# Optimization experiments

Measured on AMD Instinct MI355X. Metric: run time of the kernel, lower is better.

The kernel has to match this reference:

```python
import jax, jax.numpy as jnp
import numpy as np

B, C, N, D = 4, 128, 4096, 128  # batch, channels (=d_tran=out), points
BN_EPS = 1e-5


def setup_inputs() -> dict:
    key = jax.random.key(0)
    ks = jax.random.split(key, 10)
    s = 1.0 / np.sqrt(C)
    return {
        "x": jax.random.normal(ks[0], (B, C, N), dtype=jnp.float32),
        "Wqk": jax.random.uniform(ks[1], (D, C), minval=-s, maxval=s, dtype=jnp.float32),  # shared q/k weight
        "Wv": jax.random.uniform(ks[2], (D, C), minval=-s, maxval=s, dtype=jnp.float32),
        "bv": jax.random.uniform(ks[3], (D,), minval=-s, maxval=s, dtype=jnp.float32),
        "Wt": jax.random.uniform(ks[4], (C, D), minval=-s, maxval=s, dtype=jnp.float32),
        "bt": jax.random.uniform(ks[5], (C,), minval=-s, maxval=s, dtype=jnp.float32),
        "gamma": jnp.ones((C,), dtype=jnp.float32) + 0.1 * jax.random.normal(ks[6], (C,), dtype=jnp.float32),
        "beta": 0.1 * jax.random.normal(ks[7], (C,), dtype=jnp.float32),
        "rmean": 0.1 * jax.random.normal(ks[8], (C,), dtype=jnp.float32),
        "rvar": jax.random.uniform(ks[9], (C,), minval=0.5, maxval=1.5, dtype=jnp.float32),
    }


def reference(x, Wqk, Wv, bv, Wt, bt, gamma, beta, rmean, rvar):
    # x: [B, C, N]; 1x1 convs are per-point matmuls over the channel dim.
    x_q = jnp.einsum('dc,bcn->bnd', Wqk, x)                 # [B, N, D]
    x_k = jnp.einsum('dc,bcn->bdn', Wqk, x)                 # [B, D, N] (tied weight)
    x_v = jnp.einsum('dc,bcn->bdn', Wv, x) + bv[None, :, None]
    energy = jnp.einsum('bnd,bdm->bnm', x_q, x_k)           # [B, N, N]
    attention = jax.nn.softmax(energy, axis=-1)             # row softmax
    attention = attention / (1e-9 + attention.sum(axis=1, keepdims=True))  # L1 over columns
    x_r = jnp.einsum('bdn,bnm->bdm', x_v, attention)        # [B, D, N]
    y = jnp.einsum('od,bdn->bon', Wt, x - x_r) + bt[None, :, None]
    # BatchNorm1d, inference mode (running stats)
    y = gamma[None, :, None] * (y - rmean[None, :, None]) * jax.lax.rsqrt(rvar[None, :, None] + BN_EPS) + beta[None, :, None]
    return x + jax.nn.relu(y)
```

## Files before the change

kernel.cpp:

```cpp
#include <hip/hip_runtime.h>
#include <hip/hip_bf16.h>

typedef unsigned int u32;
typedef unsigned short u16;
using bf16x8 = __attribute__((ext_vector_type(8))) short;
using f32x4  = __attribute__((ext_vector_type(4))) float;
using f32x16 = __attribute__((ext_vector_type(16))) float;

#define B_ 4
#define C_ 128
#define N_ 4096
#define D_ 128
#define NS 8
#define NSEG (N_ / NS)

#define QS_STRIDE 136
#define VS_STRIDE 40

__device__ __forceinline__ u16 f2bf(float f) {
    u32 x = __builtin_bit_cast(u32, f);
    x = x + 0x7fffu + ((x >> 16) & 1u);
    return (u16)(x >> 16);
}
__device__ __forceinline__ float bf2f(u16 h) {
    return __builtin_bit_cast(float, (u32)h << 16);
}
__device__ __forceinline__ u32 cvtpk(float lo, float hi) {
    u32 d;
    asm("v_cvt_pk_bf16_f32 %0, %1, %2" : "=v"(d) : "v"(lo), "v"(hi));
    return d;
}
#define EXP2 __builtin_amdgcn_exp2f
__device__ __forceinline__ bf16x8 pack8(const float* v, float s) {
    bf16x8 r;
#pragma unroll
    for (int j = 0; j < 8; ++j) r[j] = (short)f2bf(v[j] * s);
    return r;
}

__global__ __launch_bounds__(256) void k_proj(
        const float* __restrict__ x, const float* __restrict__ Wqk,
        const float* __restrict__ Wv, const float* __restrict__ bv,
        u16* __restrict__ Qbf, u16* __restrict__ Vbf) {
    __shared__ float xs[C_ * 65];
    const int bid = blockIdx.x;
    const int b  = bid >> 6;
    const int n0 = (bid & 63) << 6;
    const int t  = threadIdx.x;
    const float* xb = x + (size_t)b * C_ * N_;
    for (int i = 0; i < 32; ++i) {
        int idx = i * 256 + t;
        int c = idx >> 6, n = idx & 63;
        xs[c * 65 + n] = xb[(size_t)c * N_ + n0 + n];
    }
    __syncthreads();
    const int lane = t & 63, w = t >> 6;
    const int l15 = lane & 15, g = lane >> 4;
    const float SC = 1.2011224087864498f;

    bf16x8 xf[4];
#pragma unroll
    for (int kk = 0; kk < 4; ++kk) {
        float tmp[8];
#pragma unroll
        for (int j = 0; j < 8; ++j) tmp[j] = xs[(kk * 32 + g * 8 + j) * 65 + (16 * w + l15)];
        xf[kk] = pack8(tmp, 1.0f);
    }
    for (int dt = 0; dt < 8; ++dt) {
        const int d = dt * 16 + l15;
        bf16x8 wq[4], wv[4];
#pragma unroll
        for (int kk = 0; kk < 4; ++kk) {
            const float* pq = Wqk + (size_t)d * C_ + kk * 32 + g * 8;
            const float* pv = Wv  + (size_t)d * C_ + kk * 32 + g * 8;
            float a[8], c8[8];
#pragma unroll
            for (int j = 0; j < 8; ++j) { a[j] = pq[j]; c8[j] = pv[j]; }
            wq[kk] = pack8(a, SC);
            wv[kk] = pack8(c8, 1.0f);
        }
        f32x4 aq = {0.f, 0.f, 0.f, 0.f}, av = {0.f, 0.f, 0.f, 0.f};
#pragma unroll
        for (int kk = 0; kk < 4; ++kk) {
            aq = __builtin_amdgcn_mfma_f32_16x16x32_bf16(xf[kk], wq[kk], aq, 0, 0, 0);
            av = __builtin_amdgcn_mfma_f32_16x16x32_bf16(wv[kk], xf[kk], av, 0, 0, 0);
        }
#pragma unroll
        for (int r = 0; r < 4; ++r) {
            int nn = n0 + 16 * w + g * 4 + r;
            Qbf[((size_t)b * N_ + nn) * D_ + dt * 16 + l15] = f2bf(aq[r]);
            int dd = dt * 16 + g * 4 + r;
            Vbf[((size_t)b * D_ + dd) * N_ + n0 + 16 * w + l15] = f2bf(av[r] + bv[dd]);
        }
    }
}

__global__ __launch_bounds__(256, 4) void k_pass1(const u16* __restrict__ Qbf,
                                                  float* __restrict__ rsp) {
    __shared__ __align__(16) u16 qs[32 * QS_STRIDE];
    int bid = blockIdx.x;
    const int s = bid & 7; bid >>= 3;
    const int ntile = bid & 31; const int b = bid >> 5;
    const int t = threadIdx.x, lane = t & 63, w = t >> 6;
    const int l31 = lane & 31, hi = lane >> 5;
    const int nb = ntile * 128 + w * 32;

    bf16x8 bqn[8];
    {
        const u16* qn = Qbf + ((size_t)b * N_ + nb + l31) * D_ + hi * 8;
#pragma unroll
        for (int dblk = 0; dblk < 8; ++dblk) bqn[dblk] = *(const bf16x8*)(qn + dblk * 16);
    }
    const int srow = t >> 4, sslot = t & 15;
    const u16* qsrc = Qbf + ((size_t)b * N_ + s * NSEG + srow) * D_ + sslot * 8;
    u16* qdst = qs + srow * QS_STRIDE + sslot * 8;
    uint4 qpre0 = *(const uint4*)qsrc;
    uint4 qpre1 = *(const uint4*)(qsrc + (size_t)16 * D_);

    float rs0 = 0.f, rs1 = 0.f;
    for (int mc = 0; mc < NSEG / 32; ++mc) {
        __syncthreads();
        *(uint4*)qdst = qpre0;
        *(uint4*)(qdst + 16 * QS_STRIDE) = qpre1;
        if (mc < NSEG / 32 - 1) {
            qpre0 = *(const uint4*)(qsrc + (size_t)(mc + 1) * 32 * D_);
            qpre1 = *(const uint4*)(qsrc + (size_t)((mc + 1) * 32 + 16) * D_);
        }
        __syncthreads();
        f32x16 e;
#pragma unroll
        for (int i = 0; i < 16; ++i) e[i] = 0.f;
#pragma unroll
        for (int dblk = 0; dblk < 8; ++dblk) {
            bf16x8 am = *(const bf16x8*)(qs + l31 * QS_STRIDE + (2 * dblk + hi) * 8);
            e = __builtin_amdgcn_mfma_f32_32x32x16_bf16(am, bqn[dblk], e, 0, 0, 0);
        }
#pragma unroll
        for (int r = 0; r < 16; r += 2) {
            rs0 += EXP2(e[r] - 64.0f);
            rs1 += EXP2(e[r + 1] - 64.0f);
        }
    }
    float rs = rs0 + rs1;
    rs += __shfl_xor(rs, 32);
    if (lane < 32) rsp[((size_t)s * B_ + b) * N_ + nb + l31] = rs;
}

__global__ void k_irs(const float* __restrict__ rsp, float* __restrict__ irs) {
    int i = blockIdx.x * 256 + threadIdx.x;
    if (i < B_ * N_) {
        float s = 0.f;
#pragma unroll
        for (int sp = 0; sp < NS; ++sp) s += rsp[(size_t)sp * B_ * N_ + i];
        irs[i] = 1.0f / s;
    }
}

__global__ __launch_bounds__(256, 3) void k_pass2(
        const u16* __restrict__ Qbf, const u16* __restrict__ Vbf,
        const float* __restrict__ irs, u32* __restrict__ Rp32,
        float* __restrict__ csp) {
    __shared__ __align__(16) u16 qs[32 * QS_STRIDE];
    __shared__ __align__(16) u16 vs[128 * VS_STRIDE];
    int bid = blockIdx.x;
    const int s = bid & 7; bid >>= 3;
    const int mtile = bid & 31; const int b = bid >> 5;
    const int t = threadIdx.x, lane = t & 63, w = t >> 6;
    const int l31 = lane & 31, hi = lane >> 5;
    const int m0 = mtile * 128 + w * 32;

    bf16x8 bq[8];
    {
        const u16* qm = Qbf + ((size_t)b * N_ + m0 + l31) * D_ + hi * 8;
#pragma unroll
        for (int dblk = 0; dblk < 8; ++dblk) bq[dblk] = *(const bf16x8*)(qm + dblk * 16);
    }
    f32x16 acc[4];
#pragma unroll
    for (int i = 0; i < 4; ++i)
#pragma unroll
        for (int r = 0; r < 16; ++r) acc[i][r] = 0.f;
    float cs = 0.f;
    const float* irsb = irs + (size_t)b * N_;

    const int qrow = t >> 4, qslot = t & 15;
    const u16* qsrc = Qbf + ((size_t)b * N_ + s * NSEG + qrow) * D_ + qslot * 8;
    u16* qdst = qs + qrow * QS_STRIDE + qslot * 8;
    const int vd = t >> 2, vslot = t & 3;
    const u16* vsrc = Vbf + ((size_t)b * D_ + vd) * N_ + s * NSEG + vslot * 8;
    u16* vdst = vs + vd * VS_STRIDE + vslot * 8;

    uint4 qpre0 = *(const uint4*)qsrc;
    uint4 qpre1 = *(const uint4*)(qsrc + (size_t)16 * D_);
    uint4 vpre0 = *(const uint4*)vsrc;
    uint4 vpre1 = *(const uint4*)(vsrc + (size_t)64 * N_);

    for (int nc = 0; nc < NSEG / 32; ++nc) {
        const int nb = s * NSEG + nc * 32;
        __syncthreads();
        *(uint4*)qdst = qpre0;
        *(uint4*)(qdst + 16 * QS_STRIDE) = qpre1;
        *(uint4*)vdst = vpre0;
        *(uint4*)(vdst + 64 * VS_STRIDE) = vpre1;
        if (nc < NSEG / 32 - 1) {
            qpre0 = *(const uint4*)(qsrc + (size_t)(nc + 1) * 32 * D_);
            qpre1 = *(const uint4*)(qsrc + (size_t)((nc + 1) * 32 + 16) * D_);
            vpre0 = *(const uint4*)(vsrc + (nc + 1) * 32);
            vpre1 = *(const uint4*)(vsrc + (size_t)64 * N_ + (nc + 1) * 32);
        }
        __syncthreads();

        const float* irp = irsb + nb;
        float si[32];
#pragma unroll
        for (int j = 0; j < 32; ++j) si[j] = irp[j];

        f32x16 e;
#pragma unroll
        for (int i = 0; i < 16; ++i) e[i] = 0.f;
#pragma unroll
        for (int dblk = 0; dblk < 8; ++dblk) {
            bf16x8 aq = *(const bf16x8*)(qs + l31 * QS_STRIDE + (2 * dblk + hi) * 8);
            e = __builtin_amdgcn_mfma_f32_32x32x16_bf16(aq, bq[dblk], e, 0, 0, 0);
        }
        uint4 bpA0, bpA1;
        {
            u32 A[8];
#pragma unroll
            for (int i = 0; i < 8; ++i) {
                const int c = 2 * (i & 1) + 8 * (i >> 1);
                float ir0 = hi ? si[c + 4] : si[c];
                float ir1 = hi ? si[c + 5] : si[c + 1];
                float p0 = EXP2(e[2 * i] - 64.0f) * ir0;
                float p1 = EXP2(e[2 * i + 1] - 64.0f) * ir1;
                cs += p0 + p1;
                A[i] = cvtpk(p0, p1);
            }
            u32 X0 = (u32)__shfl_xor((int)A[0], 32), X1 = (u32)__shfl_xor((int)A[1], 32);
            u32 X2 = (u32)__shfl_xor((int)A[2], 32), X3 = (u32)__shfl_xor((int)A[3], 32);
            u32 X4 = (u32)__shfl_xor((int)A[4], 32), X5 = (u32)__shfl_xor((int)A[5], 32);
            u32 X6 = (u32)__shfl_xor((int)A[6], 32), X7 = (u32)__shfl_xor((int)A[7], 32);
            bpA0 = (uint4){hi ? X2 : A[0], hi ? X3 : A[1], hi ? A[2] : X0, hi ? A[3] : X1};
            bpA1 = (uint4){hi ? X6 : A[4], hi ? X7 : A[5], hi ? A[6] : X4, hi ? A[7] : X5};
        }
#pragma unroll
        for (int nblk = 0; nblk < 2; ++nblk) {
            bf16x8 bp = __builtin_bit_cast(bf16x8, nblk ? bpA1 : bpA0);
#pragma unroll
            for (int dblk = 0; dblk < 4; ++dblk) {
                bf16x8 av = *(const bf16x8*)(vs + (dblk * 32 + l31) * VS_STRIDE +
                                             (nblk * 2 + hi) * 8);
                acc[dblk] = __builtin_amdgcn_mfma_f32_32x32x16_bf16(av, bp, acc[dblk], 0, 0, 0);
            }
        }
    }
    cs += __shfl_xor(cs, 32);
    if (lane < 32) csp[((size_t)s * B_ + b) * N_ + m0 + l31] = cs;
    u32* rpb = Rp32 + ((size_t)s * B_ + b) * (size_t)(D_ / 2) * N_;
#pragma unroll
    for (int dblk = 0; dblk < 4; ++dblk) {
#pragma unroll
        for (int j = 0; j < 8; ++j) {
            const int row = dblk * 16 + (j & 1) + 4 * (j >> 1) + 2 * hi;
            u32 pk = cvtpk(acc[dblk][2 * j], acc[dblk][2 * j + 1]);
            rpb[(size_t)row * N_ + m0 + l31] = pk;
        }
    }
}

__global__ __launch_bounds__(256) void k_final(
        const float* __restrict__ x, const float* __restrict__ Wt,
        const float* __restrict__ bt, const float* __restrict__ gamma,
        const float* __restrict__ beta, const float* __restrict__ rmean,
        const float* __restrict__ rvar, const u32* __restrict__ Rp32,
        const float* __restrict__ csp, float* __restrict__ out) {
    __shared__ float us[128 * 65];
    __shared__ float icss[64];
    const int bid = blockIdx.x;
    const int b = bid >> 6;
    const int n0 = (bid & 63) << 6;
    const int t = threadIdx.x, lane = t & 63, w = t >> 6;
    const int l15 = lane & 15, g = lane >> 4;
    if (t < 64) {
        float s = 0.f;
#pragma unroll
        for (int sp = 0; sp < NS; ++sp)
            s += csp[((size_t)sp * B_ + b) * N_ + n0 + t];
        icss[t] = 1.0f / (1e-9f + s);
    }
    __syncthreads();
    const float* xb = x + (size_t)b * C_ * N_;
    for (int i = 0; i < 16; ++i) {
        int idx = i * 256 + t;
        int dp = idx >> 6, n = idx & 63;
        float r0 = 0.f, r1 = 0.f;
#pragma unroll
        for (int sp = 0; sp < NS; ++sp) {
            u32 v = Rp32[(((size_t)(sp * B_ + b) * (D_ / 2)) + dp) * N_ + n0 + n];
            r0 += bf2f((u16)(v & 0xffffu));
            r1 += bf2f((u16)(v >> 16));
        }
        float ic = icss[n];
        us[(2 * dp) * 65 + n]     = xb[(size_t)(2 * dp) * N_ + n0 + n]     - r0 * ic;
        us[(2 * dp + 1) * 65 + n] = xb[(size_t)(2 * dp + 1) * N_ + n0 + n] - r1 * ic;
    }
    __syncthreads();
    bf16x8 uf[4];
#pragma unroll
    for (int kk = 0; kk < 4; ++kk) {
        float tmp[8];
#pragma unroll
        for (int j = 0; j < 8; ++j) tmp[j] = us[(kk * 32 + g * 8 + j) * 65 + (16 * w + l15)];
        uf[kk] = pack8(tmp, 1.0f);
    }
    for (int ct = 0; ct < 8; ++ct) {
        const int c = ct * 16 + l15;
        bf16x8 wf[4];
#pragma unroll
        for (int kk = 0; kk < 4; ++kk) {
            const float* p = Wt + (size_t)c * D_ + kk * 32 + g * 8;
            float a[8];
#pragma unroll
            for (int j = 0; j < 8; ++j) a[j] = p[j];
            wf[kk] = pack8(a, 1.0f);
        }
        f32x4 acc = {0.f, 0.f, 0.f, 0.f};
#pragma unroll
        for (int kk = 0; kk < 4; ++kk)
            acc = __builtin_amdgcn_mfma_f32_16x16x32_bf16(wf[kk], uf[kk], acc, 0, 0, 0);
#pragma unroll
        for (int r = 0; r < 4; ++r) {
            const int cc = ct * 16 + g * 4 + r;
            const int nn = n0 + 16 * w + l15;
            float y = acc[r] + bt[cc];
            float bn = gamma[cc] * (y - rmean[cc]) * rsqrtf(rvar[cc] + 1e-5f) + beta[cc];
            float rl = fmaxf(bn, 0.0f);
            out[((size_t)b * C_ + cc) * N_ + nn] = xb[(size_t)cc * N_ + nn] + rl;
        }
    }
}

extern "C" void kernel_launch(void* const* d_in, const int* in_sizes, int n_in,
                              void* d_out, int out_size, void* d_ws, size_t ws_size,
                              hipStream_t stream) {
    (void)in_sizes; (void)n_in; (void)out_size; (void)ws_size;
    const float* x     = (const float*)d_in[0];
    const float* Wqk   = (const float*)d_in[1];
    const float* Wv    = (const float*)d_in[2];
    const float* bv    = (const float*)d_in[3];
    const float* Wt    = (const float*)d_in[4];
    const float* bt    = (const float*)d_in[5];
    const float* gamma = (const float*)d_in[6];
    const float* beta  = (const float*)d_in[7];
    const float* rmean = (const float*)d_in[8];
    const float* rvar  = (const float*)d_in[9];
    float* out = (float*)d_out;

    char* ws = (char*)d_ws;
    u16*   Qbf = (u16*)(ws);
    u16*   Vbf = (u16*)(ws + 4194304);
    float* rsp = (float*)(ws + 8388608);
    float* irs = (float*)(ws + 8912896);
    float* csp = (float*)(ws + 8978432);
    u32*   Rp  = (u32*)(ws + 9502720);

    k_proj  <<<B_ * 64,      256, 0, stream>>>(x, Wqk, Wv, bv, Qbf, Vbf);
    k_pass1 <<<B_ * 32 * NS, 256, 0, stream>>>(Qbf, rsp);
    k_irs   <<<(B_ * N_ + 255) / 256, 256, 0, stream>>>(rsp, irs);
    k_pass2 <<<B_ * 32 * NS, 256, 0, stream>>>(Qbf, Vbf, irs, Rp, csp);
    k_final <<<B_ * 64,      256, 0, stream>>>(x, Wt, bt, gamma, beta, rmean, rvar, Rp, csp, out);
}
```

Measured before the change: 128.9 us.

## Double-buffer LDS tiles in attention passes, split MFMA chains, widen final kernel

```diff
diff --git a/kernel.cpp b/kernel.cpp
--- a/kernel.cpp
+++ b/kernel.cpp
@@ -97,7 +97,7 @@
 
 __global__ __launch_bounds__(256, 4) void k_pass1(const u16* __restrict__ Qbf,
                                                   float* __restrict__ rsp) {
-    __shared__ __align__(16) u16 qs[32 * QS_STRIDE];
+    __shared__ __align__(16) u16 qs[2][32 * QS_STRIDE];
     int bid = blockIdx.x;
     const int s = bid & 7; bid >>= 3;
     const int ntile = bid & 31; const int b = bid >> 5;
@@ -113,33 +113,44 @@
     }
     const int srow = t >> 4, sslot = t & 15;
     const u16* qsrc = Qbf + ((size_t)b * N_ + s * NSEG + srow) * D_ + sslot * 8;
-    u16* qdst = qs + srow * QS_STRIDE + sslot * 8;
-    uint4 qpre0 = *(const uint4*)qsrc;
-    uint4 qpre1 = *(const uint4*)(qsrc + (size_t)16 * D_);
+    const int qoff = srow * QS_STRIDE + sslot * 8;
+
+    {
+        uint4 a0 = *(const uint4*)qsrc;
+        uint4 a1 = *(const uint4*)(qsrc + (size_t)16 * D_);
+        *(uint4*)&qs[0][qoff] = a0;
+        *(uint4*)&qs[0][qoff + 16 * QS_STRIDE] = a1;
+    }
+    __syncthreads();
 
     float rs0 = 0.f, rs1 = 0.f;
     for (int mc = 0; mc < NSEG / 32; ++mc) {
-        __syncthreads();
-        *(uint4*)qdst = qpre0;
-        *(uint4*)(qdst + 16 * QS_STRIDE) = qpre1;
+        const int cur = mc & 1;
+        uint4 qpre0, qpre1;
         if (mc < NSEG / 32 - 1) {
             qpre0 = *(const uint4*)(qsrc + (size_t)(mc + 1) * 32 * D_);
             qpre1 = *(const uint4*)(qsrc + (size_t)((mc + 1) * 32 + 16) * D_);
         }
+        f32x16 ea, eb;
+#pragma unroll
+        for (int i = 0; i < 16; ++i) { ea[i] = 0.f; eb[i] = 0.f; }
+#pragma unroll
+        for (int dblk = 0; dblk < 4; ++dblk) {
+            bf16x8 am0 = *(const bf16x8*)(qs[cur] + l31 * QS_STRIDE + (2 * dblk + hi) * 8);
+            bf16x8 am1 = *(const bf16x8*)(qs[cur] + l31 * QS_STRIDE + (2 * (dblk + 4) + hi) * 8);
+            ea = __builtin_amdgcn_mfma_f32_32x32x16_bf16(am0, bqn[dblk], ea, 0, 0, 0);
+            eb = __builtin_amdgcn_mfma_f32_32x32x16_bf16(am1, bqn[dblk + 4], eb, 0, 0, 0);
+        }
+#pragma unroll
+        for (int r = 0; r < 16; r += 2) {
+            rs0 += EXP2(ea[r] + eb[r] - 64.0f);
+            rs1 += EXP2(ea[r + 1] + eb[r + 1] - 64.0f);
+        }
+        if (mc < NSEG / 32 - 1) {
+            *(uint4*)&qs[cur ^ 1][qoff] = qpre0;
+            *(uint4*)&qs[cur ^ 1][qoff + 16 * QS_STRIDE] = qpre1;
+        }
         __syncthreads();
-        f32x16 e;
-#pragma unroll
-        for (int i = 0; i < 16; ++i) e[i] = 0.f;
-#pragma unroll
-        for (int dblk = 0; dblk < 8; ++dblk) {
-            bf16x8 am = *(const bf16x8*)(qs + l31 * QS_STRIDE + (2 * dblk + hi) * 8);
-            e = __builtin_amdgcn_mfma_f32_32x32x16_bf16(am, bqn[dblk], e, 0, 0, 0);
-        }
-#pragma unroll
-        for (int r = 0; r < 16; r += 2) {
-            rs0 += EXP2(e[r] - 64.0f);
-            rs1 += EXP2(e[r + 1] - 64.0f);
-        }
     }
     float rs = rs0 + rs1;
     rs += __shfl_xor(rs, 32);
@@ -160,8 +171,8 @@
         const u16* __restrict__ Qbf, const u16* __restrict__ Vbf,
         const float* __restrict__ irs, u32* __restrict__ Rp32,
         float* __restrict__ csp) {
-    __shared__ __align__(16) u16 qs[32 * QS_STRIDE];
-    __shared__ __align__(16) u16 vs[128 * VS_STRIDE];
+    __shared__ __align__(16) u16 qs[2][32 * QS_STRIDE];
+    __shared__ __align__(16) u16 vs[2][128 * VS_STRIDE];
     int bid = blockIdx.x;
     const int s = bid & 7; bid >>= 3;
     const int mtile = bid & 31; const int b = bid >> 5;
@@ -185,43 +196,47 @@
 
     const int qrow = t >> 4, qslot = t & 15;
     const u16* qsrc = Qbf + ((size_t)b * N_ + s * NSEG + qrow) * D_ + qslot * 8;
-    u16* qdst = qs + qrow * QS_STRIDE + qslot * 8;
+    const int qoff = qrow * QS_STRIDE + qslot * 8;
     const int vd = t >> 2, vslot = t & 3;
     const u16* vsrc = Vbf + ((size_t)b * D_ + vd) * N_ + s * NSEG + vslot * 8;
-    u16* vdst = vs + vd * VS_STRIDE + vslot * 8;
-
-    uint4 qpre0 = *(const uint4*)qsrc;
-    uint4 qpre1 = *(const uint4*)(qsrc + (size_t)16 * D_);
-    uint4 vpre0 = *(const uint4*)vsrc;
-    uint4 vpre1 = *(const uint4*)(vsrc + (size_t)64 * N_);
+    const int voff = vd * VS_STRIDE + vslot * 8;
+
+    {
+        uint4 a0 = *(const uint4*)qsrc;
+        uint4 a1 = *(const uint4*)(qsrc + (size_t)16 * D_);
+        uint4 b0 = *(const uint4*)vsrc;
+        uint4 b1 = *(const uint4*)(vsrc + (size_t)64 * N_);
+        *(uint4*)&qs[0][qoff] = a0;
+        *(uint4*)&qs[0][qoff + 16 * QS_STRIDE] = a1;
+        *(uint4*)&vs[0][voff] = b0;
+        *(uint4*)&vs[0][voff + 64 * VS_STRIDE] = b1;
+    }
+    __syncthreads();
 
     for (int nc = 0; nc < NSEG / 32; ++nc) {
+        const int cur = nc & 1;
         const int nb = s * NSEG + nc * 32;
-        __syncthreads();
-        *(uint4*)qdst = qpre0;
-        *(uint4*)(qdst + 16 * QS_STRIDE) = qpre1;
-        *(uint4*)vdst = vpre0;
-        *(uint4*)(vdst + 64 * VS_STRIDE) = vpre1;
+        uint4 qpre0, qpre1, vpre0, vpre1;
         if (nc < NSEG / 32 - 1) {
             qpre0 = *(const uint4*)(qsrc + (size_t)(nc + 1) * 32 * D_);
             qpre1 = *(const uint4*)(qsrc + (size_t)((nc + 1) * 32 + 16) * D_);
             vpre0 = *(const uint4*)(vsrc + (nc + 1) * 32);
             vpre1 = *(const uint4*)(vsrc + (size_t)64 * N_ + (nc + 1) * 32);
         }
-        __syncthreads();
-
         const float* irp = irsb + nb;
         float si[32];
 #pragma unroll
         for (int j = 0; j < 32; ++j) si[j] = irp[j];
 
-        f32x16 e;
-#pragma unroll
-        for (int i = 0; i < 16; ++i) e[i] = 0.f;
-#pragma unroll
-        for (int dblk = 0; dblk < 8; ++dblk) {
-            bf16x8 aq = *(const bf16x8*)(qs + l31 * QS_STRIDE + (2 * dblk + hi) * 8);
-            e = __builtin_amdgcn_mfma_f32_32x32x16_bf16(aq, bq[dblk], e, 0, 0, 0);
+        f32x16 ea, eb;
+#pragma unroll
+        for (int i = 0; i < 16; ++i) { ea[i] = 0.f; eb[i] = 0.f; }
+#pragma unroll
+        for (int dblk = 0; dblk < 4; ++dblk) {
+            bf16x8 aq0 = *(const bf16x8*)(qs[cur] + l31 * QS_STRIDE + (2 * dblk + hi) * 8);
+            bf16x8 aq1 = *(const bf16x8*)(qs[cur] + l31 * QS_STRIDE + (2 * (dblk + 4) + hi) * 8);
+            ea = __builtin_amdgcn_mfma_f32_32x32x16_bf16(aq0, bq[dblk], ea, 0, 0, 0);
+            eb = __builtin_amdgcn_mfma_f32_32x32x16_bf16(aq1, bq[dblk + 4], eb, 0, 0, 0);
         }
         uint4 bpA0, bpA1;
         {
@@ -231,8 +246,8 @@
                 const int c = 2 * (i & 1) + 8 * (i >> 1);
                 float ir0 = hi ? si[c + 4] : si[c];
                 float ir1 = hi ? si[c + 5] : si[c + 1];
-                float p0 = EXP2(e[2 * i] - 64.0f) * ir0;
-                float p1 = EXP2(e[2 * i + 1] - 64.0f) * ir1;
+                float p0 = EXP2(ea[2 * i] + eb[2 * i] - 64.0f) * ir0;
+                float p1 = EXP2(ea[2 * i + 1] + eb[2 * i + 1] - 64.0f) * ir1;
                 cs += p0 + p1;
                 A[i] = cvtpk(p0, p1);
             }
@@ -248,11 +263,18 @@
             bf16x8 bp = __builtin_bit_cast(bf16x8, nblk ? bpA1 : bpA0);
 #pragma unroll
             for (int dblk = 0; dblk < 4; ++dblk) {
-                bf16x8 av = *(const bf16x8*)(vs + (dblk * 32 + l31) * VS_STRIDE +
+                bf16x8 av = *(const bf16x8*)(vs[cur] + (dblk * 32 + l31) * VS_STRIDE +
                                              (nblk * 2 + hi) * 8);
                 acc[dblk] = __builtin_amdgcn_mfma_f32_32x32x16_bf16(av, bp, acc[dblk], 0, 0, 0);
             }
         }
+        if (nc < NSEG / 32 - 1) {
+            *(uint4*)&qs[cur ^ 1][qoff] = qpre0;
+            *(uint4*)&qs[cur ^ 1][qoff + 16 * QS_STRIDE] = qpre1;
+            *(uint4*)&vs[cur ^ 1][voff] = vpre0;
+            *(uint4*)&vs[cur ^ 1][voff + 64 * VS_STRIDE] = vpre1;
+        }
+        __syncthreads();
     }
     cs += __shfl_xor(cs, 32);
     if (lane < 32) csp[((size_t)s * B_ + b) * N_ + m0 + l31] = cs;
@@ -268,7 +290,7 @@
     }
 }
 
-__global__ __launch_bounds__(256) void k_final(
+__global__ __launch_bounds__(512) void k_final(
         const float* __restrict__ x, const float* __restrict__ Wt,
         const float* __restrict__ bt, const float* __restrict__ gamma,
         const float* __restrict__ beta, const float* __restrict__ rmean,
@@ -290,8 +312,8 @@
     }
     __syncthreads();
     const float* xb = x + (size_t)b * C_ * N_;
-    for (int i = 0; i < 16; ++i) {
-        int idx = i * 256 + t;
+    for (int i = 0; i < 8; ++i) {
+        int idx = i * 512 + t;
         int dp = idx >> 6, n = idx & 63;
         float r0 = 0.f, r1 = 0.f;
 #pragma unroll
@@ -305,15 +327,18 @@
         us[(2 * dp + 1) * 65 + n] = xb[(size_t)(2 * dp + 1) * N_ + n0 + n] - r1 * ic;
     }
     __syncthreads();
+    const int cg = w & 3;
+    const int ct0 = (w >> 2) * 4;
     bf16x8 uf[4];
 #pragma unroll
     for (int kk = 0; kk < 4; ++kk) {
         float tmp[8];
 #pragma unroll
-        for (int j = 0; j < 8; ++j) tmp[j] = us[(kk * 32 + g * 8 + j) * 65 + (16 * w + l15)];
+        for (int j = 0; j < 8; ++j) tmp[j] = us[(kk * 32 + g * 8 + j) * 65 + (16 * cg + l15)];
         uf[kk] = pack8(tmp, 1.0f);
     }
-    for (int ct = 0; ct < 8; ++ct) {
+    for (int cti = 0; cti < 4; ++cti) {
+        const int ct = ct0 + cti;
         const int c = ct * 16 + l15;
         bf16x8 wf[4];
 #pragma unroll
@@ -331,7 +356,7 @@
 #pragma unroll
         for (int r = 0; r < 4; ++r) {
             const int cc = ct * 16 + g * 4 + r;
-            const int nn = n0 + 16 * w + l15;
+            const int nn = n0 + 16 * cg + l15;
             float y = acc[r] + bt[cc];
             float bn = gamma[cc] * (y - rmean[cc]) * rsqrtf(rvar[cc] + 1e-5f) + beta[cc];
             float rl = fmaxf(bn, 0.0f);
@@ -368,5 +393,5 @@
     k_pass1 <<<B_ * 32 * NS, 256, 0, stream>>>(Qbf, rsp);
     k_irs   <<<(B_ * N_ + 255) / 256, 256, 0, stream>>>(rsp, irs);
     k_pass2 <<<B_ * 32 * NS, 256, 0, stream>>>(Qbf, Vbf, irs, Rp, csp);
-    k_final <<<B_ * 64,      256, 0, stream>>>(x, Wt, bt, gamma, beta, rmean, rvar, Rp, csp, out);
-}
+    k_final <<<B_ * 64,      512, 0, stream>>>(x, Wt, bt, gamma, beta, rmean, rvar, Rp, csp, out);
+}
```

After: 119.7 us. 7.2% less time.
